# Optimization experiments

Measured on AMD Instinct MI355X. Metric: run time of the kernel, lower is better.

## Reference

```python
import jax, jax.numpy as jnp
import numpy as np

B, S, CTX, DIM = 2, 2048, 2048, 2048
H, HKV, HD = 16, 4, 128
HID = 5464  # 4*ceil(int(4*DIM*2/3)/4)
EPS = 1.1920929e-07  # torch eps=None -> finfo(fp32).eps
REP = H // HKV


def rmsnorm(x, w):
    return x * jax.lax.rsqrt(jnp.mean(x * x, axis=-1, keepdims=True) + EPS) * w


def rotate_half(x):
    # interleaved rotate: out[::2] = -x[1::2], out[1::2] = x[::2]
    x2 = x.reshape(x.shape[:-1] + (-1, 2))
    return jnp.stack([-x2[..., 1], x2[..., 0]], axis=-1).reshape(x.shape)


def masked_attn(q, k, v, mask):
    # q,k,v: [B,H,Sq/Sk,D]; mask broadcastable to [B,H,Sq,Sk]
    scale = 1.0 / jnp.sqrt(jnp.asarray(q.shape[-1], q.dtype))
    s = jnp.einsum('bhqd,bhkd->bhqk', q, k) * scale
    s = jnp.where(mask, s, jnp.asarray(-1e30, s.dtype))
    p = jax.nn.softmax(s, axis=-1)
    p = jnp.where(mask, p, 0.0)  # fully-masked rows -> 0 output (flex_attention semantics)
    return jnp.einsum('bhqk,bhkd->bhqd', p, v)


def setup_inputs() -> dict:
    key = jax.random.key(0)
    ks = jax.random.split(key, 20)
    std = 0.02
    return {
        'x': jax.random.normal(ks[0], (B, S, DIM), jnp.float32),
        'context': jax.random.normal(ks[1], (B, CTX, DIM), jnp.float32),
        'freqs_cos': jax.random.uniform(ks[2], (S, 1, HD), jnp.float32),
        'freqs_sin': jax.random.uniform(ks[3], (S, 1, HD), jnp.float32),
        'wqkv': jax.random.normal(ks[4], ((H + 2 * HKV) * HD, DIM), jnp.float32) * std,
        'wo_self': jax.random.normal(ks[5], (DIM, DIM), jnp.float32) * std,
        'qn_self': jnp.ones((HD,), jnp.float32),
        'kn_self': jnp.ones((HD,), jnp.float32),
        'wq': jax.random.normal(ks[6], (H * HD, DIM), jnp.float32) * std,
        'wkv': jax.random.normal(ks[7], (2 * HKV * HD, DIM), jnp.float32) * std,
        'wo_cross': jax.random.normal(ks[8], (DIM, DIM), jnp.float32) * std,
        'qn_cross': jnp.ones((HD,), jnp.float32),
        'kn_cross': jnp.ones((HD,), jnp.float32),
        'w1': jax.random.normal(ks[9], (HID, DIM), jnp.float32) * std,
        'w2': jax.random.normal(ks[10], (DIM, HID), jnp.float32) * std,
        'attn_norm_w': jnp.ones((DIM,), jnp.float32),
        'cross_norm_w': jnp.ones((DIM,), jnp.float32),
        'ffn_norm_w': jnp.ones((DIM,), jnp.float32),
        'vis_mask': jax.random.randint(ks[11], (B, S), 0, 2).astype(bool),
        'context_mask': jax.random.randint(ks[12], (B, CTX), 0, 2).astype(bool),
    }


def reference(x, context, freqs_cos, freqs_sin, wqkv, wo_self, qn_self, kn_self,
              wq, wkv, wo_cross, qn_cross, kn_cross, w1, w2,
              attn_norm_w, cross_norm_w, ffn_norm_w, vis_mask, context_mask):
    b, s, _ = x.shape
    ctx = context.shape[1]

    # ---- self-attention (prenorm) ----
    h0 = rmsnorm(x, attn_norm_w)
    qkv = h0 @ wqkv.T
    xq = qkv[..., :H * HD].reshape(b, s, H, HD)
    xk = qkv[..., H * HD:(H + HKV) * HD].reshape(b, s, HKV, HD)
    xv = qkv[..., (H + HKV) * HD:].reshape(b, s, HKV, HD)
    xq = rmsnorm(xq, qn_self)   # qk-norm BEFORE rope in self-attn
    xk = rmsnorm(xk, kn_self)
    xq = xq * freqs_cos + rotate_half(xq) * freqs_sin
    xk = xk * freqs_cos + rotate_half(xk) * freqs_sin
    q = xq.transpose(0, 2, 1, 3)
    k = jnp.repeat(xk.transpose(0, 2, 1, 3), REP, axis=1)
    v = jnp.repeat(xv.transpose(0, 2, 1, 3), REP, axis=1)
    m_self = vis_mask[:, None, :, None] & vis_mask[:, None, None, :]
    a = masked_attn(q, k, v, m_self)
    h = x + a.transpose(0, 2, 1, 3).reshape(b, s, DIM) @ wo_self.T

    # ---- cross-attention (prenorm) ----
    hc = rmsnorm(h, cross_norm_w)
    xq = (hc @ wq.T).reshape(b, s, H, HD)
    kv = context @ wkv.T
    xk = kv[..., :HKV * HD].reshape(b, ctx, HKV, HD)
    xv = kv[..., HKV * HD:].reshape(b, ctx, HKV, HD)
    xq = xq * freqs_cos + rotate_half(xq) * freqs_sin  # rope on q BEFORE qk-norm in cross-attn
    xq = rmsnorm(xq, qn_cross)
    xk = rmsnorm(xk, kn_cross)
    q = xq.transpose(0, 2, 1, 3)
    k = jnp.repeat(xk.transpose(0, 2, 1, 3), REP, axis=1)
    v = jnp.repeat(xv.transpose(0, 2, 1, 3), REP, axis=1)
    m_cross = context_mask[:, None, None, :]
    a = masked_attn(q, k, v, m_cross)
    h = h + a.transpose(0, 2, 1, 3).reshape(b, s, DIM) @ wo_cross.T

    # ---- FFN (silu) ----
    hf = rmsnorm(h, ffn_norm_w)
    return h + jax.nn.silu(hf @ w1.T) @ w2.T
```

## Files before the change

### kernel.cpp

```cpp
#include <hip/hip_runtime.h>

#define DEVI __device__ __forceinline__

typedef __attribute__((ext_vector_type(4))) float f32x4;
typedef __attribute__((ext_vector_type(8))) __bf16 bf16x8;

static constexpr float EPS = 1.1920929e-07f;
static constexpr float SC2L = 0.12751551960234575f;

DEVI float bf2f(unsigned short u){ return __uint_as_float(((unsigned)u)<<16); }
DEVI unsigned short f2bfu(float f){
  unsigned u = __float_as_uint(f);
  u += 0x7fffu + ((u>>16)&1u);
  return (unsigned short)(u>>16);
}
DEVI unsigned pack2(float a, float b){ return (unsigned)f2bfu(a) | ((unsigned)f2bfu(b)<<16); }
DEVI float exp2a(float x){ float r; asm("v_exp_f32 %0, %1" : "=v"(r) : "v"(x)); return r; }
DEVI unsigned cvtpk(float lo, float hi){
  unsigned r; asm("v_cvt_pk_bf16_f32 %0, %1, %2" : "=v"(r) : "v"(lo), "v"(hi)); return r;
}

DEVI void gload16(const void* g, const void* l){
  __builtin_amdgcn_global_load_lds((const __attribute__((address_space(1))) void*)g,
                                   (__attribute__((address_space(3))) void*)l, 16, 0, 0);
}

__global__ void k_masknorm(const unsigned* __restrict__ vin, const unsigned* __restrict__ cin,
                           unsigned char* __restrict__ vout, unsigned char* __restrict__ cout){
  __shared__ int smode;
  const int t = threadIdx.x;
  if (t==0) smode = 0;
  __syncthreads();
  unsigned loc = 0;
  for (int i=t; i<1024; i+=256) loc |= (vin[i] > 1u);
  if (loc) smode = 1;
  __syncthreads();
  if (smode){
    for (int i=t; i<1024; i+=256){
      ((unsigned*)vout)[i] = vin[i];
      ((unsigned*)cout)[i] = cin[i];
    }
  } else {
    const int* vi = (const int*)vin; const int* ci = (const int*)cin;
    for (int i=t; i<4096; i+=256){
      vout[i] = (unsigned char)(vi[i] != 0);
      cout[i] = (unsigned char)(ci[i] != 0);
    }
  }
}

__global__ void k_conv(const float* __restrict__ s, unsigned short* __restrict__ d, int n4){
  int i = blockIdx.x*256 + threadIdx.x;
  if (i >= n4) return;
  float4 v = ((const float4*)s)[i];
  uint2 u; u.x = pack2(v.x, v.y); u.y = pack2(v.z, v.w);
  ((uint2*)d)[i] = u;
}
__global__ void k_convpad_rows(const float* __restrict__ s, unsigned short* __restrict__ d,
                               int R, int C, int Rp){
  int i = blockIdx.x*256 + threadIdx.x;
  int total = (Rp*C)>>2;
  if (i >= total) return;
  uint2 u; u.x = 0u; u.y = 0u;
  if (i*4 < R*C){ float4 v = ((const float4*)s)[i]; u.x = pack2(v.x,v.y); u.y = pack2(v.z,v.w); }
  ((uint2*)d)[i] = u;
}
__global__ void k_convpad_cols(const float* __restrict__ s, unsigned short* __restrict__ d,
                               int N, int K, int Kp){
  int i = blockIdx.x*256 + threadIdx.x;
  int total = (N*Kp)>>2;
  if (i >= total) return;
  int i4 = i*4; int n = i4/Kp; int k = i4 - n*Kp;
  uint2 u; u.x = 0u; u.y = 0u;
  if (k < K){ float4 v = *(const float4*)(s + (size_t)n*K + k); u.x = pack2(v.x,v.y); u.y = pack2(v.z,v.w); }
  ((uint2*)d)[i] = u;
}

__global__ void k_rms(const float* __restrict__ X, const float* __restrict__ W,
                      unsigned short* __restrict__ Y){
  const int row = blockIdx.x, tid = threadIdx.x;
  const float* x = X + (size_t)row*2048;
  float4 v0 = ((const float4*)x)[tid*2];
  float4 v1 = ((const float4*)x)[tid*2+1];
  float ss = v0.x*v0.x+v0.y*v0.y+v0.z*v0.z+v0.w*v0.w
           + v1.x*v1.x+v1.y*v1.y+v1.z*v1.z+v1.w*v1.w;
  #pragma unroll
  for (int o=32;o;o>>=1) ss += __shfl_xor(ss, o);
  __shared__ float red[4];
  if ((tid&63)==0) red[tid>>6] = ss;
  __syncthreads();
  float tot = red[0]+red[1]+red[2]+red[3];
  float rs = rsqrtf(tot*(1.0f/2048.0f) + EPS);
  float4 w0 = ((const float4*)W)[tid*2];
  float4 w1 = ((const float4*)W)[tid*2+1];
  uint4 u;
  u.x = pack2(v0.x*rs*w0.x, v0.y*rs*w0.y);
  u.y = pack2(v0.z*rs*w0.z, v0.w*rs*w0.w);
  u.z = pack2(v1.x*rs*w1.x, v1.y*rs*w1.y);
  u.w = pack2(v1.z*rs*w1.z, v1.w*rs*w1.w);
  *(uint4*)(Y + (size_t)row*2048 + tid*8) = u;
}

template<int EPI>
__global__ void k_gemm(const unsigned short* __restrict__ A, const unsigned short* __restrict__ Bw,
                       void* Cout, const float* resid, int M, int N, int K){
  __shared__ __align__(16) unsigned short sm[16384];
  const int tid = threadIdx.x;
  const int w = tid>>6, l = tid&63, g = l>>4, q = l&15;
  const int bm = blockIdx.y<<7, bn = blockIdx.x<<7;
  const int wr = (w>>1)<<6, wc = (w&1)<<6;
  f32x4 acc[4][4];
  #pragma unroll
  for (int a=0;a<4;++a)
    #pragma unroll
    for (int b2=0;b2<4;++b2) acc[a][b2] = f32x4{0.f,0.f,0.f,0.f};

  const unsigned short* Ag = A + (size_t)bm*K;
  const unsigned short* Bg = Bw + (size_t)bn*K;
  const int nk = K>>5;
  int cur = 0;

  auto STAGE = [&](int buf, int kt){
    #pragma unroll
    for (int i=0;i<2;++i){
      int L = (i*256+tid)*16;
      int r = L>>6; int ce = (L&63)>>1;
      int lofs = __builtin_amdgcn_readfirstlane(buf*8192 + i*4096 + (tid>>6)*1024);
      gload16(Ag + (size_t)r*K + (kt<<5) + ce, (const char*)sm + lofs);
    }
    #pragma unroll
    for (int i=0;i<2;++i){
      int L = (i*256+tid)*16;
      int r = L>>6; int ce = (L&63)>>1;
      int lofs = __builtin_amdgcn_readfirstlane(16384 + buf*8192 + i*4096 + (tid>>6)*1024);
      gload16(Bg + (size_t)r*K + (kt<<5) + ce, (const char*)sm + lofs);
    }
  };

  STAGE(0, 0);
  __syncthreads();
  for (int kt=0; kt<nk; ++kt){
    if (kt+1 < nk) STAGE(cur^1, kt+1);
    const unsigned short* Ab = sm + cur*4096;
    const unsigned short* Bb = sm + 8192 + cur*4096;
    bf16x8 af[4], bfr[4];
    #pragma unroll
    for (int mi=0;mi<4;++mi) af[mi] = *(const bf16x8*)(Ab + (wr + mi*16 + q)*32 + g*8);
    #pragma unroll
    for (int ni=0;ni<4;++ni) bfr[ni] = *(const bf16x8*)(Bb + (wc + ni*16 + q)*32 + g*8);
    #pragma unroll
    for (int mi=0;mi<4;++mi)
      #pragma unroll
      for (int ni=0;ni<4;++ni)
        acc[mi][ni] = __builtin_amdgcn_mfma_f32_16x16x32_bf16(af[mi], bfr[ni], acc[mi][ni], 0,0,0);
    __syncthreads();
    cur ^= 1;
  }
  #pragma unroll
  for (int mi=0;mi<4;++mi)
    #pragma unroll
    for (int ni=0;ni<4;++ni)
      #pragma unroll
      for (int r=0;r<4;++r){
        int row = bm + wr + mi*16 + g*4 + r;
        int col = bn + wc + ni*16 + q;
        size_t idx = (size_t)row*N + col;
        float v = acc[mi][ni][r];
        if (EPI==0) ((unsigned short*)Cout)[idx] = f2bfu(v);
        else if (EPI==1){ float sg = v/(1.0f+__expf(-v)); ((unsigned short*)Cout)[idx] = f2bfu(sg); }
        else ((float*)Cout)[idx] = resid[idx] + v;
      }
}

template<int EPI>
__global__ __launch_bounds__(512,1)
void k_gemm2(const unsigned short* __restrict__ A, const unsigned short* __restrict__ Bw,
             void* Cout, const float* resid, int M, int N, int K){
  __shared__ __align__(16) char sm[147456];
  const int tid = threadIdx.x;
  const int wid = tid>>6, l = tid&63, g = l>>4, q = l&15;
  const int wm = wid>>2, wn = wid&3;
  const int bm = blockIdx.y<<7, bn = blockIdx.x<<8;
  f32x4 acc[4][4];
  #pragma unroll
  for (int a=0;a<4;++a)
    #pragma unroll
    for (int b2=0;b2<4;++b2) acc[a][b2] = f32x4{0.f,0.f,0.f,0.f};

  const unsigned short* Ag = A + (size_t)bm*K;
  const unsigned short* Bg = Bw + (size_t)bn*K;
  const int nk = K>>6;

  auto STAGE_A = [&](int buf, int kt){
    #pragma unroll
    for (int j=0;j<2;++j){
      int L = (j*512+tid)*16;
      int lr = L>>7, c8 = (L>>4)&7;
      int cg = c8 ^ (lr&7);
      int lofs = __builtin_amdgcn_readfirstlane(buf*49152 + j*8192 + wid*1024);
      gload16(Ag + (size_t)lr*K + (kt<<6) + cg*8, sm + lofs);
    }
  };
  auto STAGE_B1 = [&](int buf, int kt, int j){
    int L = (j*512+tid)*16;
    int rn = L>>7, c8 = (L>>4)&7;
    int cg = c8 ^ (rn&7);
    int lofs = __builtin_amdgcn_readfirstlane(buf*49152 + 16384 + j*8192 + wid*1024);
    gload16(Bg + (size_t)rn*K + (kt<<6) + cg*8, sm + lofs);
  };

  STAGE_A(0,0); STAGE_B1(0,0,0); STAGE_B1(0,0,1); STAGE_B1(0,0,2); STAGE_B1(0,0,3);
  STAGE_A(1,1); STAGE_B1(1,1,0); STAGE_B1(1,1,1); STAGE_B1(1,1,2); STAGE_B1(1,1,3);

  int buf = 0;
  for (int kt=0; kt<nk; ++kt){
    int p2 = buf+2; if (p2>2) p2-=3;
    if (kt+1 < nk) asm volatile("s_waitcnt vmcnt(6)" ::: "memory");
    else           asm volatile("s_waitcnt vmcnt(0)" ::: "memory");
    asm volatile("s_waitcnt lgkmcnt(0)" ::: "memory");
    __builtin_amdgcn_s_barrier();
    asm volatile("" ::: "memory");

    const char* Ab = sm + buf*49152;
    const char* Bb = sm + buf*49152 + 16384;

    #pragma unroll
    for (int ks=0; ks<2; ++ks){
      if (kt+2 < nk){
        if (ks==0){ STAGE_A(p2, kt+2); STAGE_B1(p2, kt+2, 0); }
        else      { STAGE_B1(p2, kt+2, 1); STAGE_B1(p2, kt+2, 2); STAGE_B1(p2, kt+2, 3); }
      }
      bf16x8 af[4], bfr[4];
      #pragma unroll
      for (int mi=0;mi<4;++mi){
        int lr = wm*64 + mi*16 + q;
        af[mi] = *(const bf16x8*)(Ab + lr*128 + (((ks*4+g) ^ (lr&7))<<4));
      }
      #pragma unroll
      for (int ni=0;ni<4;++ni){
        int rn = wn*64 + ni*16 + q;
        bfr[ni] = *(const bf16x8*)(Bb + rn*128 + (((ks*4+g) ^ (rn&7))<<4));
      }
      asm volatile("s_waitcnt lgkmcnt(0)" ::: "memory");
      __builtin_amdgcn_s_setprio(1);
      #pragma unroll
      for (int mi=0;mi<4;++mi)
        #pragma unroll
        for (int ni=0;ni<4;++ni)
          acc[mi][ni] = __builtin_amdgcn_mfma_f32_16x16x32_bf16(af[mi], bfr[ni], acc[mi][ni], 0,0,0);
      __builtin_amdgcn_s_setprio(0);
    }
    buf = (buf==2) ? 0 : buf+1;
  }

  #pragma unroll
  for (int mi=0;mi<4;++mi)
    #pragma unroll
    for (int ni=0;ni<4;++ni)
      #pragma unroll
      for (int r=0;r<4;++r){
        int row = bm + wm*64 + mi*16 + g*4 + r;
        int col = bn + wn*64 + ni*16 + q;
        size_t idx = (size_t)row*N + col;
        float v = acc[mi][ni][r];
        if (EPI==0) ((unsigned short*)Cout)[idx] = f2bfu(v);
        else if (EPI==1){ float sg = v/(1.0f+__expf(-v)); ((unsigned short*)Cout)[idx] = f2bfu(sg); }
        else ((float*)Cout)[idx] = resid[idx] + v;
      }
}

__global__ void k_self_pp(const unsigned short* __restrict__ qkv, const float* __restrict__ fc,
                          const float* __restrict__ fs, const float* __restrict__ qn,
                          const float* __restrict__ kn,
                          unsigned short* __restrict__ Qb, unsigned short* __restrict__ Kb,
                          unsigned short* __restrict__ Vt){
  const int row = blockIdx.x;
  const int b = row>>11, s = row&2047;
  const int w = threadIdx.x>>6, l = threadIdx.x&63;
  const int d0 = 2*l, d1 = d0+1;
  const float c0 = fc[s*128+d0], c1 = fc[s*128+d1];
  const float s0 = fs[s*128+d0], s1 = fs[s*128+d1];
  #pragma unroll
  for (int it=0; it<6; ++it){
    const int hh = it*4 + w;
    const unsigned short* src = qkv + (size_t)row*3072 + hh*128;
    if (hh >= 20){
      const int hv = hh - 20;
      size_t base = ((size_t)(b*4 + hv))*128*2048;
      Vt[base + (size_t)d0*2048 + s] = src[d0];
      Vt[base + (size_t)d1*2048 + s] = src[d1];
    } else {
      float x0 = bf2f(src[d0]), x1 = bf2f(src[d1]);
      float ss = x0*x0 + x1*x1;
      #pragma unroll
      for (int o=32;o;o>>=1) ss += __shfl_xor(ss, o);
      float rs = rsqrtf(ss*(1.0f/128.0f) + EPS);
      if (hh < 16){
        float y0 = x0*rs*qn[d0], y1 = x1*rs*qn[d1];
        *(unsigned*)(Qb + (((size_t)(b*16 + hh)*2048 + s)*128) + d0)
          = pack2((y0*c0 - y1*s0)*SC2L, (y1*c1 + y0*s1)*SC2L);
      } else {
        float y0 = x0*rs*kn[d0], y1 = x1*rs*kn[d1];
        *(unsigned*)(Kb + (((size_t)(b*4 + (hh-16))*2048 + s)*128) + d0)
          = pack2(y0*c0 - y1*s0, y1*c1 + y0*s1);
      }
    }
  }
}

__global__ void k_crossq_pp(const unsigned short* __restrict__ qc, const float* __restrict__ fc,
                            const float* __restrict__ fs, const float* __restrict__ qn,
                            unsigned short* __restrict__ Qb){
  const int row = blockIdx.x;
  const int b = row>>11, s = row&2047;
  const int w = threadIdx.x>>6, l = threadIdx.x&63;
  const int d0 = 2*l, d1 = d0+1;
  const float c0 = fc[s*128+d0], c1 = fc[s*128+d1];
  const float s0 = fs[s*128+d0], s1 = fs[s*128+d1];
  #pragma unroll
  for (int it=0; it<4; ++it){
    const int hh = it*4 + w;
    const unsigned short* src = qc + (size_t)row*2048 + hh*128;
    float x0 = bf2f(src[d0]), x1 = bf2f(src[d1]);
    float y0 = x0*c0 - x1*s0;
    float y1 = x1*c1 + x0*s1;
    float ss = y0*y0 + y1*y1;
    #pragma unroll
    for (int o=32;o;o>>=1) ss += __shfl_xor(ss, o);
    float rs = rsqrtf(ss*(1.0f/128.0f) + EPS);
    *(unsigned*)(Qb + (((size_t)(b*16 + hh)*2048 + s)*128) + d0)
      = pack2(y0*rs*qn[d0]*SC2L, y1*rs*qn[d1]*SC2L);
  }
}

__global__ void k_crosskv_pp(const unsigned short* __restrict__ kvc, const float* __restrict__ kn,
                             unsigned short* __restrict__ Kb, unsigned short* __restrict__ Vt){
  const int row = blockIdx.x;
  const int b = row>>11, s = row&2047;
  const int w = threadIdx.x>>6, l = threadIdx.x&63;
  const int d0 = 2*l, d1 = d0+1;
  #pragma unroll
  for (int it=0; it<2; ++it){
    const int hh = it*4 + w;
    const unsigned short* src = kvc + (size_t)row*1024 + hh*128;
    if (hh < 4){
      float x0 = bf2f(src[d0]), x1 = bf2f(src[d1]);
      float ss = x0*x0 + x1*x1;
      #pragma unroll
      for (int o=32;o;o>>=1) ss += __shfl_xor(ss, o);
      float rs = rsqrtf(ss*(1.0f/128.0f) + EPS);
      *(unsigned*)(Kb + (((size_t)(b*4 + hh)*2048 + s)*128) + d0)
        = pack2(x0*rs*kn[d0], x1*rs*kn[d1]);
    } else {
      const int hv = hh-4;
      size_t base = ((size_t)(b*4 + hv))*128*2048;
      Vt[base + (size_t)d0*2048 + s] = src[d0];
      Vt[base + (size_t)d1*2048 + s] = src[d1];
    }
  }
}

template<bool QMASK>
__global__ void k_attn(const unsigned short* __restrict__ Qg, const unsigned short* __restrict__ Kg,
                       const unsigned short* __restrict__ Vtg,
                       const unsigned char* __restrict__ qm, const unsigned char* __restrict__ km,
                       unsigned short* __restrict__ Og, int H, int HKV){
  constexpr int SK = 2048, SQ = 2048, NT = SK/64;
  __shared__ __align__(16) char smem[81920];
  const int qt = blockIdx.x, h = blockIdx.y, b = blockIdx.z;
  const int hk = h / (H/HKV);
  const int tid = threadIdx.x, w = tid>>6, l = tid&63, g = l>>4, q = l&15;

  {
    const unsigned long long mv = ((const unsigned long long*)(km + (size_t)b*SK))[tid];
    float* bl = (float*)(smem + 73728);
    #pragma unroll
    for (int j=0;j<8;++j)
      bl[tid*8+j] = ((mv>>(8*j)) & 0xffull) ? 0.0f : -3.0e38f;
  }

  const size_t qrow = (size_t)(b*H + h)*SQ + qt*64 + w*16 + q;
  bf16x8 qf[4];
  #pragma unroll
  for (int ks=0;ks<4;++ks) qf[ks] = *(const bf16x8*)(Qg + qrow*128 + ks*32 + g*8);

  f32x4 oacc[8];
  #pragma unroll
  for (int i=0;i<8;++i) oacc[i] = f32x4{0.f,0.f,0.f,0.f};
  float m_run = -1.0e30f, l_run = 0.f;

  const unsigned short* Kt0 = Kg + (size_t)(b*HKV + hk)*SK*128;
  const unsigned short* Vt0 = Vtg + (size_t)(b*HKV + hk)*128*SK;
  const float* biasf = (const float*)(smem + 73728);
  char* Pl = smem + 65536 + w*2048;

  auto STAGE_T = [&](int t, int p){
    #pragma unroll
    for (int i=0;i<4;++i){
      int L = (i*256+tid)*16;
      int r = L>>8, c16 = (L>>4)&15;
      int c = (c16 & 8) | ((c16 & 7) ^ (r & 7));
      int lofs = __builtin_amdgcn_readfirstlane(p*16384 + i*4096 + w*1024);
      gload16(Kt0 + (size_t)(t*64 + r)*128 + c*8, smem + lofs);
    }
    #pragma unroll
    for (int i=0;i<4;++i){
      int L = (i*256+tid)*16;
      int d = L>>7, c8 = (L>>4)&7;
      int c = c8 ^ (d & 7);
      int lofs = __builtin_amdgcn_readfirstlane(32768 + p*16384 + i*4096 + w*1024);
      gload16(Vt0 + (size_t)d*SK + t*64 + c*8, smem + lofs);
    }
  };

  STAGE_T(0, 0);

  for (int t=0; t<NT; ++t){
    const int p = t&1;
    asm volatile("s_waitcnt lgkmcnt(0)" ::: "memory");
    __builtin_amdgcn_s_barrier();
    asm volatile("" ::: "memory");
    if (t+1 < NT){
      STAGE_T(t+1, p^1);
      asm volatile("s_waitcnt vmcnt(8)" ::: "memory");
    } else {
      asm volatile("s_waitcnt vmcnt(0)" ::: "memory");
    }
    __builtin_amdgcn_s_barrier();
    asm volatile("" ::: "memory");

    const char* Kb_ = smem + p*16384;
    const char* Vb_ = smem + 32768 + p*16384;

    f32x4 sacc[4];
    #pragma unroll
    for (int i=0;i<4;++i) sacc[i] = f32x4{0.f,0.f,0.f,0.f};
    __builtin_amdgcn_s_setprio(1);
    #pragma unroll
    for (int ks=0;ks<4;++ks){
      #pragma unroll
      for (int mi=0;mi<4;++mi){
        int kcol = mi*16 + q;
        int c = 4*ks + g;
        int c16 = (c & 8) | ((c & 7) ^ (kcol & 7));
        bf16x8 ak = *(const bf16x8*)(Kb_ + kcol*256 + c16*16);
        sacc[mi] = __builtin_amdgcn_mfma_f32_16x16x32_bf16(ak, qf[ks], sacc[mi], 0,0,0);
      }
    }
    __builtin_amdgcn_s_setprio(0);

    float sv[4][4];
    float mloc = -3.0e38f;
    #pragma unroll
    for (int mi=0;mi<4;++mi){
      f32x4 bb = *(const f32x4*)(biasf + t*64 + mi*16 + g*4);
      #pragma unroll
      for (int r=0;r<4;++r){
        float v = sacc[mi][r] + bb[r];
        sv[mi][r] = v;
        mloc = fmaxf(mloc, v);
      }
    }
    mloc = fmaxf(mloc, __shfl_xor(mloc, 16));
    mloc = fmaxf(mloc, __shfl_xor(mloc, 32));
    if (!__all(mloc - m_run <= 8.0f)){
      float mnew = fmaxf(m_run, mloc);
      float alpha = exp2a(m_run - mnew);
      l_run *= alpha;
      #pragma unroll
      for (int i=0;i<8;++i) oacc[i] *= alpha;
      m_run = mnew;
    }
    float rsum = 0.f;
    unsigned pb[4][2];
    #pragma unroll
    for (int mi=0;mi<4;++mi){
      float p0 = exp2a(sv[mi][0] - m_run);
      float p1 = exp2a(sv[mi][1] - m_run);
      float p2 = exp2a(sv[mi][2] - m_run);
      float p3 = exp2a(sv[mi][3] - m_run);
      rsum += (p0+p1)+(p2+p3);
      pb[mi][0] = cvtpk(p0, p1);
      pb[mi][1] = cvtpk(p2, p3);
    }
    rsum += __shfl_xor(rsum, 16);
    rsum += __shfl_xor(rsum, 32);
    l_run += rsum;

    #pragma unroll
    for (int mi=0;mi<4;++mi){
      int c16 = (2*mi + (g>>1)) ^ (q & 7);
      uint2 uu; uu.x = pb[mi][0]; uu.y = pb[mi][1];
      *(uint2*)(Pl + q*128 + c16*16 + (g&1)*8) = uu;
    }
    asm volatile("" ::: "memory");

    __builtin_amdgcn_s_setprio(1);
    #pragma unroll
    for (int ks=0;ks<2;++ks){
      int c16 = (4*ks + g) ^ (q & 7);
      bf16x8 pf = *(const bf16x8*)(Pl + q*128 + c16*16);
      #pragma unroll
      for (int mi=0;mi<8;++mi){
        int d = mi*16 + q;
        bf16x8 vf = *(const bf16x8*)(Vb_ + d*128 + c16*16);
        oacc[mi] = __builtin_amdgcn_mfma_f32_16x16x32_bf16(vf, pf, oacc[mi], 0,0,0);
      }
    }
    __builtin_amdgcn_s_setprio(0);
  }

  float inv = (l_run > 0.f) ? 1.0f/l_run : 0.f;
  if (QMASK){
    if (!qm[(size_t)b*SQ + qt*64 + w*16 + q]) inv = 0.f;
  }
  __syncthreads();
  float* Ot = (float*)smem;
  #pragma unroll
  for (int mi=0;mi<8;++mi)
    #pragma unroll
    for (int r=0;r<4;++r){
      int d = mi*16 + g*4 + r;
      Ot[d*65 + w*16 + q] = oacc[mi][r]*inv;
    }
  __syncthreads();
  int qloc = tid>>2, seg = tid&3;
  int srow = qt*64 + qloc;
  size_t obase = ((size_t)b*SQ + srow)*(size_t)(H*128) + (size_t)h*128 + seg*32;
  #pragma unroll
  for (int p4=0;p4<4;++p4){
    float vv[8];
    #pragma unroll
    for (int j=0;j<8;++j) vv[j] = Ot[(seg*32 + p4*8 + j)*65 + qloc];
    uint4 u;
    u.x = pack2(vv[0],vv[1]); u.y = pack2(vv[2],vv[3]);
    u.z = pack2(vv[4],vv[5]); u.w = pack2(vv[6],vv[7]);
    *(uint4*)(Og + obase + p4*8) = u;
  }
}

extern "C" void kernel_launch(void* const* d_in, const int* in_sizes, int n_in,
                              void* d_out, int out_size, void* d_ws, size_t ws_size,
                              hipStream_t stream){
  const float* x        = (const float*)d_in[0];
  const float* ctx      = (const float*)d_in[1];
  const float* fc       = (const float*)d_in[2];
  const float* fs       = (const float*)d_in[3];
  const float* wqkv     = (const float*)d_in[4];
  const float* wo_self  = (const float*)d_in[5];
  const float* qn_self  = (const float*)d_in[6];
  const float* kn_self  = (const float*)d_in[7];
  const float* wq       = (const float*)d_in[8];
  const float* wkv      = (const float*)d_in[9];
  const float* wo_cross = (const float*)d_in[10];
  const float* qn_cross = (const float*)d_in[11];
  const float* kn_cross = (const float*)d_in[12];
  const float* w1       = (const float*)d_in[13];
  const float* w2       = (const float*)d_in[14];
  const float* attn_nw  = (const float*)d_in[15];
  const float* cross_nw = (const float*)d_in[16];
  const float* ffn_nw   = (const float*)d_in[17];
  const unsigned* vis_raw   = (const unsigned*)d_in[18];
  const unsigned* cmask_raw = (const unsigned*)d_in[19];
  float* out = (float*)d_out;

  char* ws = (char*)d_ws;
  unsigned short* wslot = (unsigned short*)(ws);
  unsigned short* ctxbf = (unsigned short*)(ws +  23068672);
  unsigned short* nbuf  = (unsigned short*)(ws +  39845888);
  unsigned short* qkvb  = (unsigned short*)(ws +  56623104);
  unsigned short* Qb    = (unsigned short*)(ws +  81788928);
  unsigned short* Kb    = (unsigned short*)(ws +  98566144);
  unsigned short* Vtb   = (unsigned short*)(ws + 102760448);
  unsigned short* aob   = (unsigned short*)(ws + 106954752);
  unsigned short* midb  = (unsigned short*)(ws + 106954752);
  unsigned char*  visN  = (unsigned char*)(ws + 153092096);
  unsigned char*  cmkN  = (unsigned char*)(ws + 153096192);
  unsigned short* qcb   = qkvb;
  unsigned short* kvcb  = qkvb + 8388608;

  auto conv = [&](const float* s, unsigned short* dst, size_t n){
    int n4 = (int)(n>>2);
    k_conv<<<(n4+255)/256, 256, 0, stream>>>(s, dst, n4);
  };

  k_masknorm<<<1,256,0,stream>>>(vis_raw, cmask_raw, visN, cmkN);

  conv(ctx, ctxbf, (size_t)4096*2048);
  k_rms<<<4096,256,0,stream>>>(x, attn_nw, nbuf);
  conv(wqkv, wslot, (size_t)3072*2048);
  k_gemm2<0><<<dim3(12,32),512,0,stream>>>(nbuf, wslot, qkvb, nullptr, 4096,3072,2048);
  k_self_pp<<<4096,256,0,stream>>>(qkvb, fc, fs, qn_self, kn_self, Qb, Kb, Vtb);
  k_attn<true><<<dim3(32,16,2),256,0,stream>>>(Qb, Kb, Vtb, visN, visN, aob, 16, 4);
  conv(wo_self, wslot, (size_t)2048*2048);
  k_gemm2<2><<<dim3(8,32),512,0,stream>>>(aob, wslot, out, x, 4096,2048,2048);

  k_rms<<<4096,256,0,stream>>>(out, cross_nw, nbuf);
  conv(wq, wslot, (size_t)2048*2048);
  k_gemm2<0><<<dim3(8,32),512,0,stream>>>(nbuf, wslot, qcb, nullptr, 4096,2048,2048);
  conv(wkv, wslot, (size_t)1024*2048);
  k_gemm<0><<<dim3(8,32),256,0,stream>>>(ctxbf, wslot, kvcb, nullptr, 4096,1024,2048);
  k_crossq_pp<<<4096,256,0,stream>>>(qcb, fc, fs, qn_cross, Qb);
  k_crosskv_pp<<<4096,256,0,stream>>>(kvcb, kn_cross, Kb, Vtb);
  k_attn<false><<<dim3(32,16,2),256,0,stream>>>(Qb, Kb, Vtb, nullptr, cmkN, aob, 16, 4);
  conv(wo_cross, wslot, (size_t)2048*2048);
  k_gemm2<2><<<dim3(8,32),512,0,stream>>>(aob, wslot, out, out, 4096,2048,2048);

  k_rms<<<4096,256,0,stream>>>(out, ffn_nw, nbuf);
  k_convpad_rows<<<(5632*2048/4+255)/256,256,0,stream>>>(w1, wslot, 5464, 2048, 5632);
  k_gemm2<1><<<dim3(22,32),512,0,stream>>>(nbuf, wslot, midb, nullptr, 4096,5632,2048);
  k_convpad_cols<<<(2048*5632/4+255)/256,256,0,stream>>>(w2, wslot, 2048, 5464, 5632);
  k_gemm2<2><<<dim3(8,32),512,0,stream>>>(midb, wslot, out, out, 4096,2048,5632);

  (void)in_sizes; (void)n_in; (void)out_size; (void)ws_size;
}
```

Measured before the change: 826.9 us.

## Share K/V tiles across all query heads of a GQA group in one block

The attention kernel now launches 1024-thread blocks, one per KV head, with four query heads per block. Each K/V tile is staged into shared memory once and reused by all four heads, where before four separate blocks each loaded it. This cuts global and L2 traffic for K/V by the GQA factor. In exchange there are far fewer blocks (256 instead of 1024), a larger shared-memory footprint, and a serialized four-phase output writeback with extra barriers, which may reduce occupancy and latency hiding.

```diff
diff --git a/kernel.cpp b/kernel.cpp
--- a/kernel.cpp
+++ b/kernel.cpp
@@ -361,25 +361,28 @@
 }
 
 template<bool QMASK>
-__global__ void k_attn(const unsigned short* __restrict__ Qg, const unsigned short* __restrict__ Kg,
-                       const unsigned short* __restrict__ Vtg,
-                       const unsigned char* __restrict__ qm, const unsigned char* __restrict__ km,
-                       unsigned short* __restrict__ Og, int H, int HKV){
+__global__ __launch_bounds__(1024,1)
+void k_attn(const unsigned short* __restrict__ Qg, const unsigned short* __restrict__ Kg,
+            const unsigned short* __restrict__ Vtg,
+            const unsigned char* __restrict__ qm, const unsigned char* __restrict__ km,
+            unsigned short* __restrict__ Og, int H, int HKV){
   constexpr int SK = 2048, SQ = 2048, NT = SK/64;
-  __shared__ __align__(16) char smem[81920];
-  const int qt = blockIdx.x, h = blockIdx.y, b = blockIdx.z;
-  const int hk = h / (H/HKV);
+  __shared__ __align__(16) char smem[106496];
+  const int qt = blockIdx.x, hk = blockIdx.y, b = blockIdx.z;
+  const int REP = H/HKV;
   const int tid = threadIdx.x, w = tid>>6, l = tid&63, g = l>>4, q = l&15;
-
-  {
+  const int hq = w>>2, wsub = w&3;
+
+  if (tid < 256){
     const unsigned long long mv = ((const unsigned long long*)(km + (size_t)b*SK))[tid];
-    float* bl = (float*)(smem + 73728);
+    float* bl = (float*)(smem + 98304);
     #pragma unroll
     for (int j=0;j<8;++j)
       bl[tid*8+j] = ((mv>>(8*j)) & 0xffull) ? 0.0f : -3.0e38f;
   }
 
-  const size_t qrow = (size_t)(b*H + h)*SQ + qt*64 + w*16 + q;
+  const int h = hk*REP + hq;
+  const size_t qrow = (size_t)(b*H + h)*SQ + qt*64 + wsub*16 + q;
   bf16x8 qf[4];
   #pragma unroll
   for (int ks=0;ks<4;++ks) qf[ks] = *(const bf16x8*)(Qg + qrow*128 + ks*32 + g*8);
@@ -391,24 +394,20 @@
 
   const unsigned short* Kt0 = Kg + (size_t)(b*HKV + hk)*SK*128;
   const unsigned short* Vt0 = Vtg + (size_t)(b*HKV + hk)*128*SK;
-  const float* biasf = (const float*)(smem + 73728);
+  const float* biasf = (const float*)(smem + 98304);
   char* Pl = smem + 65536 + w*2048;
 
   auto STAGE_T = [&](int t, int p){
-    #pragma unroll
-    for (int i=0;i<4;++i){
-      int L = (i*256+tid)*16;
-      int r = L>>8, c16 = (L>>4)&15;
+    {
+      int r = tid>>4, c16 = tid&15;
       int c = (c16 & 8) | ((c16 & 7) ^ (r & 7));
-      int lofs = __builtin_amdgcn_readfirstlane(p*16384 + i*4096 + w*1024);
+      int lofs = __builtin_amdgcn_readfirstlane(p*16384 + w*1024);
       gload16(Kt0 + (size_t)(t*64 + r)*128 + c*8, smem + lofs);
     }
-    #pragma unroll
-    for (int i=0;i<4;++i){
-      int L = (i*256+tid)*16;
-      int d = L>>7, c8 = (L>>4)&7;
+    {
+      int d = tid>>3, c8 = tid&7;
       int c = c8 ^ (d & 7);
-      int lofs = __builtin_amdgcn_readfirstlane(32768 + p*16384 + i*4096 + w*1024);
+      int lofs = __builtin_amdgcn_readfirstlane(32768 + p*16384 + w*1024);
       gload16(Vt0 + (size_t)d*SK + t*64 + c*8, smem + lofs);
     }
   };
@@ -422,7 +421,7 @@
     asm volatile("" ::: "memory");
     if (t+1 < NT){
       STAGE_T(t+1, p^1);
-      asm volatile("s_waitcnt vmcnt(8)" ::: "memory");
+      asm volatile("s_waitcnt vmcnt(2)" ::: "memory");
     } else {
       asm volatile("s_waitcnt vmcnt(0)" ::: "memory");
     }
@@ -512,30 +511,32 @@
 
   float inv = (l_run > 0.f) ? 1.0f/l_run : 0.f;
   if (QMASK){
-    if (!qm[(size_t)b*SQ + qt*64 + w*16 + q]) inv = 0.f;
-  }
-  __syncthreads();
+    if (!qm[(size_t)b*SQ + qt*64 + wsub*16 + q]) inv = 0.f;
+  }
   float* Ot = (float*)smem;
-  #pragma unroll
-  for (int mi=0;mi<8;++mi)
-    #pragma unroll
-    for (int r=0;r<4;++r){
-      int d = mi*16 + g*4 + r;
-      Ot[d*65 + w*16 + q] = oacc[mi][r]*inv;
-    }
-  __syncthreads();
-  int qloc = tid>>2, seg = tid&3;
-  int srow = qt*64 + qloc;
-  size_t obase = ((size_t)b*SQ + srow)*(size_t)(H*128) + (size_t)h*128 + seg*32;
-  #pragma unroll
-  for (int p4=0;p4<4;++p4){
+  const int qloc = tid>>4, seg = tid&15;
+  #pragma unroll
+  for (int ph=0; ph<4; ++ph){
+    __syncthreads();
+    if (hq == ph){
+      #pragma unroll
+      for (int mi=0;mi<8;++mi)
+        #pragma unroll
+        for (int r=0;r<4;++r){
+          int d = mi*16 + g*4 + r;
+          Ot[d*65 + wsub*16 + q] = oacc[mi][r]*inv;
+        }
+    }
+    __syncthreads();
+    int srow = qt*64 + qloc;
+    size_t obase = ((size_t)b*SQ + srow)*(size_t)(H*128) + (size_t)(hk*REP + ph)*128 + seg*8;
     float vv[8];
     #pragma unroll
-    for (int j=0;j<8;++j) vv[j] = Ot[(seg*32 + p4*8 + j)*65 + qloc];
+    for (int j=0;j<8;++j) vv[j] = Ot[(seg*8 + j)*65 + qloc];
     uint4 u;
     u.x = pack2(vv[0],vv[1]); u.y = pack2(vv[2],vv[3]);
     u.z = pack2(vv[4],vv[5]); u.w = pack2(vv[6],vv[7]);
-    *(uint4*)(Og + obase + p4*8) = u;
+    *(uint4*)(Og + obase) = u;
   }
 }
 
@@ -591,7 +592,7 @@
   conv(wqkv, wslot, (size_t)3072*2048);
   k_gemm2<0><<<dim3(12,32),512,0,stream>>>(nbuf, wslot, qkvb, nullptr, 4096,3072,2048);
   k_self_pp<<<4096,256,0,stream>>>(qkvb, fc, fs, qn_self, kn_self, Qb, Kb, Vtb);
-  k_attn<true><<<dim3(32,16,2),256,0,stream>>>(Qb, Kb, Vtb, visN, visN, aob, 16, 4);
+  k_attn<true><<<dim3(32,4,2),1024,0,stream>>>(Qb, Kb, Vtb, visN, visN, aob, 16, 4);
   conv(wo_self, wslot, (size_t)2048*2048);
   k_gemm2<2><<<dim3(8,32),512,0,stream>>>(aob, wslot, out, x, 4096,2048,2048);
 
@@ -602,7 +603,7 @@
   k_gemm<0><<<dim3(8,32),256,0,stream>>>(ctxbf, wslot, kvcb, nullptr, 4096,1024,2048);
   k_crossq_pp<<<4096,256,0,stream>>>(qcb, fc, fs, qn_cross, Qb);
   k_crosskv_pp<<<4096,256,0,stream>>>(kvcb, kn_cross, Kb, Vtb);
-  k_attn<false><<<dim3(32,16,2),256,0,stream>>>(Qb, Kb, Vtb, nullptr, cmkN, aob, 16, 4);
+  k_attn<false><<<dim3(32,4,2),1024,0,stream>>>(Qb, Kb, Vtb, nullptr, cmkN, aob, 16, 4);
   conv(wo_cross, wslot, (size_t)2048*2048);
   k_gemm2<2><<<dim3(8,32),512,0,stream>>>(aob, wslot, out, out, 4096,2048,2048);
 
```

Result: faster. 765.9 us (-7.4%).
